# Optimization experiments

Measured on AMD Instinct MI355X. Metric: run time of the kernel, lower is better.

The kernel has to match this reference:

```python
import jax, jax.numpy as jnp
import numpy as np

DEPTH = 6
DIM = 512
HEADS = 8
HD = DIM // HEADS          # head_dim = 64
HALF = HD // 4             # RoPE2D half_dim = 16
N = 85                     # 1 CLS + 4 + 16 + 64
TOKENS = [1, 4, 16, 64]
MAX_FREQ = 10.0
NEG = -1e30


def _build_mask():
    bounds = np.cumsum([0] + TOKENS)
    M = np.array([[1, 0, 0, 1], [1, 1, 0, 0], [1, 0, 1, 0], [0, 0, 0, 1]])
    m = np.full((N, N), NEG, np.float32)
    for i in range(4):
        for j in range(4):
            if M[i, j]:
                m[bounds[i]:bounds[i + 1], bounds[j]:bounds[j + 1]] = 0.0
    return jnp.asarray(m)

MASK = _build_mask()
FREQS = jnp.exp(jnp.arange(HALF, dtype=jnp.float32) * (-np.log(MAX_FREQ) / HALF))


def _centers():
    allc = []
    for g in (2, 4, 8):
        step = 1.0 / g
        off = step / 2
        ys, xs = np.meshgrid(np.arange(g), np.arange(g), indexing='ij')
        c = np.stack([off + xs * step, off + ys * step], axis=-1).reshape(-1, 2)
        allc.append(c)
    return jnp.asarray(np.concatenate(allc, 0), dtype=jnp.float32)


def _ln(x, w, b):
    mu = x.mean(-1, keepdims=True)
    var = x.var(-1, keepdims=True)
    return (x - mu) / jnp.sqrt(var + 1e-5) * w + b


def _rope(t, coords):
    # t: [B, H, M, HD] patch tokens (CLS excluded); coords: [M, 2]
    two_pi = 2.0 * jnp.pi
    ang_x = coords[:, 0:1] * FREQS[None, :] * two_pi   # [M, HALF]
    ang_y = coords[:, 1:2] * FREQS[None, :] * two_pi
    cx, sx = jnp.cos(ang_x), jnp.sin(ang_x)
    cy, sy = jnp.cos(ang_y), jnp.sin(ang_y)
    t = t.reshape(t.shape[:-1] + (4, HALF))
    x0, x1, x2, x3 = t[..., 0, :], t[..., 1, :], t[..., 2, :], t[..., 3, :]
    r = jnp.stack([x0 * cx - x1 * sx, x0 * sx + x1 * cx,
                   x2 * cy - x3 * sy, x2 * sy + x3 * cy], axis=-2)
    return r.reshape(r.shape[:-2] + (HD,))


def _attn(x, coords, qkv_w, qkv_b, proj_w, proj_b):
    B = x.shape[0]
    qkv = (x @ qkv_w + qkv_b).reshape(B, N, 3, HEADS, HD).transpose(2, 0, 3, 1, 4)
    q, k, v = qkv[0], qkv[1], qkv[2]   # each [B, H, N, HD]
    q = jnp.concatenate([q[:, :, :1], _rope(q[:, :, 1:], coords)], axis=2)
    k = jnp.concatenate([k[:, :, :1], _rope(k[:, :, 1:], coords)], axis=2)
    scores = jnp.einsum('bhqd,bhkd->bhqk', q, k) * (HD ** -0.5) + MASK
    a = jax.nn.softmax(scores, axis=-1)
    out = jnp.einsum('bhqk,bhkd->bhqd', a, v).transpose(0, 2, 1, 3).reshape(B, N, DIM)
    return out @ proj_w + proj_b


def _forward(x, coords, ln1_w, ln1_b, qkv_w, qkv_b, proj_w, proj_b,
             ln2_w, ln2_b, fc1_w, fc1_b, fc2_w, fc2_b, lnf_w, lnf_b):
    for l in range(DEPTH):
        h = _ln(x, ln1_w[l], ln1_b[l])
        x = x + _attn(h, coords, qkv_w[l], qkv_b[l], proj_w[l], proj_b[l])
        h = _ln(x, ln2_w[l], ln2_b[l])
        h = jax.nn.gelu(h @ fc1_w[l] + fc1_b[l], approximate=False)  # torch nn.GELU = erf
        x = x + h @ fc2_w[l] + fc2_b[l]
    return _ln(x, lnf_w, lnf_b)


def setup_inputs() -> dict:
    key = jax.random.key(0)
    ks = jax.random.split(key, 5)
    B = 512
    def w(k, shape, s=0.02):
        return jax.random.normal(k, shape, jnp.float32) * s
    return {
        'x': jax.random.normal(ks[0], (B, N, DIM), jnp.float32),
        'coords': _centers(),
        'ln1_w': jnp.ones((DEPTH, DIM), jnp.float32),
        'ln1_b': jnp.zeros((DEPTH, DIM), jnp.float32),
        'qkv_w': w(ks[1], (DEPTH, DIM, 3 * DIM)),
        'qkv_b': jnp.zeros((DEPTH, 3 * DIM), jnp.float32),
        'proj_w': w(ks[2], (DEPTH, DIM, DIM)),
        'proj_b': jnp.zeros((DEPTH, DIM), jnp.float32),
        'ln2_w': jnp.ones((DEPTH, DIM), jnp.float32),
        'ln2_b': jnp.zeros((DEPTH, DIM), jnp.float32),
        'fc1_w': w(ks[3], (DEPTH, DIM, 4 * DIM)),
        'fc1_b': jnp.zeros((DEPTH, 4 * DIM), jnp.float32),
        'fc2_w': w(ks[4], (DEPTH, 4 * DIM, DIM)),
        'fc2_b': jnp.zeros((DEPTH, DIM), jnp.float32),
        'lnf_w': jnp.ones((DIM,), jnp.float32),
        'lnf_b': jnp.zeros((DIM,), jnp.float32),
    }


def reference(x, coords, ln1_w, ln1_b, qkv_w, qkv_b, proj_w, proj_b,
              ln2_w, ln2_b, fc1_w, fc1_b, fc2_w, fc2_b, lnf_w, lnf_b):
    return _forward(x, coords, ln1_w, ln1_b, qkv_w, qkv_b, proj_w, proj_b,
                    ln2_w, ln2_b, fc1_w, fc1_b, fc2_w, fc2_b, lnf_w, lnf_b)
```

## Files before the change

kernel.cpp:

```cpp
#include <hip/hip_runtime.h>
#include <hip/hip_bf16.h>

typedef unsigned short u16;
typedef unsigned int u32;
typedef __attribute__((ext_vector_type(8))) short short8;
typedef __attribute__((ext_vector_type(4))) float floatx4;

#define MTOT 43520
#define DIMM 512
#define NHEAD 8

__device__ __forceinline__ float b2f(u16 u) { return __uint_as_float(((unsigned)u) << 16); }
__device__ __forceinline__ u16 f2b(float f) {
  unsigned u = __float_as_uint(f);
  return (u16)((u + 0x7FFFu + ((u >> 16) & 1u)) >> 16);
}

__device__ __forceinline__ void gld16(void* lds, const void* g) {
  __builtin_amdgcn_global_load_lds(
      (const __attribute__((address_space(1))) u32*)g,
      (__attribute__((address_space(3))) u32*)lds, 16, 0, 0);
}

__global__ __launch_bounds__(256) void transpose_conv(const float* __restrict__ in,
    u16* __restrict__ out, int K, int N)
{
  const float* W  = in  + (size_t)blockIdx.z * K * N;
  u16*         Wt = out + (size_t)blockIdx.z * K * N;
  int n0 = blockIdx.x * 64, k0 = blockIdx.y * 64;
  int t = threadIdx.x;
  #pragma unroll
  for (int i = 0; i < 2; i++) {
    int task = t + i * 256;
    int n = task >> 3, kc = (task & 7) * 8;
    u16 tmp[8];
    #pragma unroll
    for (int j = 0; j < 8; j++)
      tmp[j] = f2b(W[(size_t)(k0 + kc + j) * N + n0 + n]);
    *(uint4*)&Wt[(size_t)(n0 + n) * K + k0 + kc] = *(uint4*)tmp;
  }
}

template<int OUTF32>
__global__ __launch_bounds__(256) void ln_kernel(const float* __restrict__ x,
    const float* __restrict__ w, const float* __restrict__ b, void* __restrict__ out)
{
  int row  = blockIdx.x * 4 + (threadIdx.x >> 6);
  int lane = threadIdx.x & 63;
  const float* xr = x + (size_t)row * DIMM;
  float4 a = ((const float4*)xr)[lane * 2];
  float4 c = ((const float4*)xr)[lane * 2 + 1];
  float f[8] = { a.x, a.y, a.z, a.w, c.x, c.y, c.z, c.w };

  float s = 0.f, ss = 0.f;
  #pragma unroll
  for (int i = 0; i < 8; i++) { s += f[i]; ss += f[i] * f[i]; }
  #pragma unroll
  for (int off = 32; off > 0; off >>= 1) {
    s  += __shfl_xor(s,  off);
    ss += __shfl_xor(ss, off);
  }
  float mu  = s * (1.f / 512.f);
  float var = ss * (1.f / 512.f) - mu * mu;
  float rs  = rsqrtf(var + 1e-5f);

  float4 w0 = ((const float4*)w)[lane * 2], w1 = ((const float4*)w)[lane * 2 + 1];
  float4 b0 = ((const float4*)b)[lane * 2], b1 = ((const float4*)b)[lane * 2 + 1];
  float wv[8] = { w0.x, w0.y, w0.z, w0.w, w1.x, w1.y, w1.z, w1.w };
  float bv[8] = { b0.x, b0.y, b0.z, b0.w, b1.x, b1.y, b1.z, b1.w };

  if (OUTF32) {
    float res[8];
    #pragma unroll
    for (int i = 0; i < 8; i++) res[i] = (f[i] - mu) * rs * wv[i] + bv[i];
    float* orow = (float*)out + (size_t)row * DIMM;
    ((float4*)orow)[lane * 2]     = *(float4*)&res[0];
    ((float4*)orow)[lane * 2 + 1] = *(float4*)&res[4];
  } else {
    u16 res[8];
    #pragma unroll
    for (int i = 0; i < 8; i++) res[i] = f2b((f[i] - mu) * rs * wv[i] + bv[i]);
    ((uint4*)((u16*)out + (size_t)row * DIMM))[lane] = *(uint4*)res;
  }
}

template<int EPI>
__global__ __launch_bounds__(256) void gemm_nt(
    const u16* __restrict__ A, const u16* __restrict__ Bt,
    const float* __restrict__ bias, const float* __restrict__ resid,
    void* __restrict__ Cv, int Nd, int K)
{
  __shared__ u16 As[128 * 32];
  __shared__ u16 Bs[128 * 32];

  int t = threadIdx.x;
  int m0 = blockIdx.y * 128, n0 = blockIdx.x * 128;
  int wave = t >> 6, lane = t & 63, quad = lane >> 4, l16 = lane & 15;
  int wr = wave >> 1, wc = wave & 1;

  floatx4 zero = {0.f, 0.f, 0.f, 0.f};
  floatx4 acc[4][4];
  #pragma unroll
  for (int mt = 0; mt < 4; mt++)
    #pragma unroll
    for (int nt = 0; nt < 4; nt++) acc[mt][nt] = zero;

  int srow = wave * 32 + (lane >> 2);
  int kch  = (lane & 3) * 8;

  for (int k0 = 0; k0 < K; k0 += 32) {
    #pragma unroll
    for (int i = 0; i < 2; i++) {
      int row = srow + i * 16;
      gld16(&As[(wave * 32 + i * 16) * 32], A  + (size_t)(m0 + row) * K + k0 + kch);
      gld16(&Bs[(wave * 32 + i * 16) * 32], Bt + (size_t)(n0 + row) * K + k0 + kch);
    }
    __syncthreads();

    short8 af[4];
    #pragma unroll
    for (int mt = 0; mt < 4; mt++)
      af[mt] = *(const short8*)&As[(wr * 64 + mt * 16 + l16) * 32 + quad * 8];
    #pragma unroll
    for (int nt = 0; nt < 4; nt++) {
      short8 bf = *(const short8*)&Bs[(wc * 64 + nt * 16 + l16) * 32 + quad * 8];
      #pragma unroll
      for (int mt = 0; mt < 4; mt++)
        acc[mt][nt] = __builtin_amdgcn_mfma_f32_16x16x32_bf16(af[mt], bf, acc[mt][nt], 0, 0, 0);
    }
    __syncthreads();
  }

  #pragma unroll
  for (int mt = 0; mt < 4; mt++) {
    #pragma unroll
    for (int nt = 0; nt < 4; nt++) {
      int nc = n0 + wc * 64 + nt * 16 + l16;
      float bv = bias[nc];
      #pragma unroll
      for (int r = 0; r < 4; r++) {
        int mr = m0 + wr * 64 + mt * 16 + quad * 4 + r;
        size_t idx = (size_t)mr * Nd + nc;
        float v = acc[mt][nt][r] + bv;
        if constexpr (EPI == 1) {
          ((float*)Cv)[idx] = v + resid[idx];
        } else if constexpr (EPI == 2) {
          v = 0.5f * v * (1.f + erff(v * 0.70710678118654752f));
          ((u16*)Cv)[idx] = f2b(v);
        } else {
          ((u16*)Cv)[idx] = f2b(v);
        }
      }
    }
  }
}

__device__ __forceinline__ int grp(int tk) { return tk == 0 ? 0 : (tk < 5 ? 1 : (tk < 21 ? 2 : 3)); }

__global__ __launch_bounds__(256) void attn_kernel(const u16* __restrict__ qkv,
    const float* __restrict__ coords, u16* __restrict__ out)
{
  __shared__ u16 Qs[96 * 72];
  __shared__ u16 Ks[96 * 72];
  __shared__ u16 Vt[64 * 104];
  __shared__ u16 Pb[96 * 104];

  int b = blockIdx.x >> 3, h = blockIdx.x & 7;
  int tid = threadIdx.x;
  const u16* base = qkv + ((size_t)b * 85) * 1536 + h * 64;

  for (int idx = tid; idx < 96 * 64; idx += 256) {
    int tk = idx >> 6, d = idx & 63;
    float qv = 0.f, kv = 0.f; u16 vv = 0;
    if (tk < 85) {
      const u16* qp = base + (size_t)tk * 1536;
      vv = qp[1024 + d];
      if (tk == 0) {
        qv = b2f(qp[d]); kv = b2f(qp[512 + d]);
      } else {
        int j = d & 15, q4 = d >> 4;
        float coord = coords[(tk - 1) * 2 + (q4 >> 1)];
        float freq = __expf((float)j * -0.14391156831212787f);
        float ang = coord * freq * 6.283185307179586f;
        float sn, cs; __sincosf(ang, &sn, &cs);
        int p0 = ((q4 & 2) << 4) + j, p1 = p0 + 16;
        float a0 = b2f(qp[p0]),       a1 = b2f(qp[p1]);
        float k0 = b2f(qp[512 + p0]), k1 = b2f(qp[512 + p1]);
        if (q4 & 1) { qv = a0 * sn + a1 * cs; kv = k0 * sn + k1 * cs; }
        else        { qv = a0 * cs - a1 * sn; kv = k0 * cs - k1 * sn; }
      }
    }
    Qs[tk * 72 + d] = f2b(qv);
    Ks[tk * 72 + d] = f2b(kv);
    Vt[d * 104 + tk] = vv;
  }
  __syncthreads();

  int wave = tid >> 6, lane = tid & 63, quad = lane >> 4, l16 = lane & 15;
  const unsigned MBITS = 0x8539u;
  floatx4 zero = {0.f, 0.f, 0.f, 0.f};

  int nb = (wave < 2) ? 2 : 1;
  for (int bi = 0; bi < nb; bi++) {
    int band = (bi == 0) ? wave : wave + 4;

    short8 a0 = *(const short8*)&Qs[(band * 16 + l16) * 72 + quad * 8];
    short8 a1 = *(const short8*)&Qs[(band * 16 + l16) * 72 + 32 + quad * 8];
    floatx4 s[6];
    #pragma unroll
    for (int nt = 0; nt < 6; nt++) {
      short8 b0 = *(const short8*)&Ks[(nt * 16 + l16) * 72 + quad * 8];
      short8 b1 = *(const short8*)&Ks[(nt * 16 + l16) * 72 + 32 + quad * 8];
      floatx4 tmp = __builtin_amdgcn_mfma_f32_16x16x32_bf16(a0, b0, zero, 0, 0, 0);
      s[nt] = __builtin_amdgcn_mfma_f32_16x16x32_bf16(a1, b1, tmp, 0, 0, 0);
    }

    int rb = band * 16 + quad * 4;
    #pragma unroll
    for (int r = 0; r < 4; r++) {
      int row = rb + r, gr = grp(row);
      float mx = -3.4e38f;
      #pragma unroll
      for (int nt = 0; nt < 6; nt++) {
        int col = nt * 16 + l16;
        float m = (col < 85 && ((MBITS >> (gr * 4 + grp(col))) & 1)) ? 0.f : -1e30f;
        s[nt][r] = s[nt][r] * 0.125f + m;
        mx = fmaxf(mx, s[nt][r]);
      }
      #pragma unroll
      for (int off = 1; off < 16; off <<= 1) mx = fmaxf(mx, __shfl_xor(mx, off));
      float sum = 0.f;
      #pragma unroll
      for (int nt = 0; nt < 6; nt++) { s[nt][r] = __expf(s[nt][r] - mx); sum += s[nt][r]; }
      #pragma unroll
      for (int off = 1; off < 16; off <<= 1) sum += __shfl_xor(sum, off);
      float inv = 1.f / sum;
      #pragma unroll
      for (int nt = 0; nt < 6; nt++)
        Pb[row * 104 + nt * 16 + l16] = f2b(s[nt][r] * inv);
    }

    floatx4 o[4];
    #pragma unroll
    for (int nt2 = 0; nt2 < 4; nt2++) o[nt2] = zero;
    #pragma unroll
    for (int ks = 0; ks < 3; ks++) {
      short8 pa = *(const short8*)&Pb[(band * 16 + l16) * 104 + ks * 32 + quad * 8];
      #pragma unroll
      for (int nt2 = 0; nt2 < 4; nt2++) {
        short8 vb = *(const short8*)&Vt[(nt2 * 16 + l16) * 104 + ks * 32 + quad * 8];
        o[nt2] = __builtin_amdgcn_mfma_f32_16x16x32_bf16(pa, vb, o[nt2], 0, 0, 0);
      }
    }
    #pragma unroll
    for (int nt2 = 0; nt2 < 4; nt2++) {
      #pragma unroll
      for (int r = 0; r < 4; r++) {
        int row = rb + r;
        if (row < 85)
          out[((size_t)b * 85 + row) * 512 + h * 64 + nt2 * 16 + l16] = f2b(o[nt2][r]);
      }
    }
  }
}

extern "C" void kernel_launch(void* const* d_in, const int* in_sizes, int n_in,
                              void* d_out, int out_size, void* d_ws, size_t ws_size,
                              hipStream_t stream) {
  (void)in_sizes; (void)n_in; (void)out_size; (void)ws_size;
  const float* x_in   = (const float*)d_in[0];
  const float* coords = (const float*)d_in[1];
  const float* ln1_w  = (const float*)d_in[2];
  const float* ln1_b  = (const float*)d_in[3];
  const float* qkv_w  = (const float*)d_in[4];
  const float* qkv_b  = (const float*)d_in[5];
  const float* proj_w = (const float*)d_in[6];
  const float* proj_b = (const float*)d_in[7];
  const float* ln2_w  = (const float*)d_in[8];
  const float* ln2_b  = (const float*)d_in[9];
  const float* fc1_w  = (const float*)d_in[10];
  const float* fc1_b  = (const float*)d_in[11];
  const float* fc2_w  = (const float*)d_in[12];
  const float* fc2_b  = (const float*)d_in[13];
  const float* lnf_w  = (const float*)d_in[14];
  const float* lnf_b  = (const float*)d_in[15];

  float* xb = (float*)d_ws;
  u16*   hb = (u16*)(xb + (size_t)MTOT * 512);
  u16*   qb = hb + (size_t)MTOT * 512;
  u16*   wbuf = qb + (size_t)MTOT * 2048;
  u16* wq = wbuf;
  u16* wp = wq + (size_t)6 * 512 * 1536;
  u16* w1 = wp + (size_t)6 * 512 * 512;
  u16* w2 = w1 + (size_t)6 * 512 * 2048;

  dim3 blk(256);
  transpose_conv<<<dim3(1536 / 64, 512 / 64, 6), blk, 0, stream>>>(qkv_w, wq, 512, 1536);
  transpose_conv<<<dim3(512 / 64, 512 / 64, 6), blk, 0, stream>>>(proj_w, wp, 512, 512);
  transpose_conv<<<dim3(2048 / 64, 512 / 64, 6), blk, 0, stream>>>(fc1_w, w1, 512, 2048);
  transpose_conv<<<dim3(512 / 64, 2048 / 64, 6), blk, 0, stream>>>(fc2_w, w2, 2048, 512);

  for (int l = 0; l < 6; l++) {
    const float* xcur = (l == 0) ? x_in : xb;
    ln_kernel<0><<<MTOT / 4, blk, 0, stream>>>(xcur, ln1_w + l * 512, ln1_b + l * 512, hb);
    gemm_nt<0><<<dim3(1536 / 128, MTOT / 128), blk, 0, stream>>>(
        hb, wq + (size_t)l * 512 * 1536, qkv_b + (size_t)l * 1536, nullptr, qb, 1536, 512);
    attn_kernel<<<512 * NHEAD, blk, 0, stream>>>(qb, coords, hb);
    gemm_nt<1><<<dim3(512 / 128, MTOT / 128), blk, 0, stream>>>(
        hb, wp + (size_t)l * 512 * 512, proj_b + (size_t)l * 512, xcur, xb, 512, 512);
    ln_kernel<0><<<MTOT / 4, blk, 0, stream>>>(xb, ln2_w + l * 512, ln2_b + l * 512, hb);
    gemm_nt<2><<<dim3(2048 / 128, MTOT / 128), blk, 0, stream>>>(
        hb, w1 + (size_t)l * 512 * 2048, fc1_b + (size_t)l * 2048, nullptr, qb, 2048, 512);
    gemm_nt<1><<<dim3(512 / 128, MTOT / 128), blk, 0, stream>>>(
        qb, w2 + (size_t)l * 2048 * 512, fc2_b + (size_t)l * 512, xb, xb, 512, 2048);
  }
  ln_kernel<1><<<MTOT / 4, blk, 0, stream>>>(xb, lnf_w, lnf_b, d_out);
}
```

Before: 4.386 ms.

## Replace 128x128 GEMM with 256x256 double-buffered, swizzled, XCD-remapped MFMA kernel

Result: faster. 4.240 ms (-3.3%).

```diff
diff --git a/kernel.cpp b/kernel.cpp
--- a/kernel.cpp
+++ b/kernel.cpp
@@ -85,61 +85,150 @@
 }
 
 template<int EPI>
-__global__ __launch_bounds__(256) void gemm_nt(
+__global__ __launch_bounds__(512, 2) void gemm256(
     const u16* __restrict__ A, const u16* __restrict__ Bt,
     const float* __restrict__ bias, const float* __restrict__ resid,
-    void* __restrict__ Cv, int Nd, int K)
+    void* __restrict__ Cv, int Nd, int K, int gx)
 {
-  __shared__ u16 As[128 * 32];
-  __shared__ u16 Bs[128 * 32];
+  __shared__ u16 As[2][2][128][64];
+  __shared__ u16 Bs[2][2][128][64];
+
+  int nwg  = gridDim.x;
+  int orig = blockIdx.x;
+  int xcd = orig & 7, cidx = orig >> 3;
+  int qq = nwg >> 3, rr8 = nwg & 7;
+  int nid = (xcd < rr8 ? xcd * (qq + 1) : rr8 * (qq + 1) + (xcd - rr8) * qq) + cidx;
+  int bx = nid % gx, by = nid / gx;
+  int m0 = by * 256, n0 = bx * 256;
 
   int t = threadIdx.x;
-  int m0 = blockIdx.y * 128, n0 = blockIdx.x * 128;
-  int wave = t >> 6, lane = t & 63, quad = lane >> 4, l16 = lane & 15;
-  int wr = wave >> 1, wc = wave & 1;
+  int w = t >> 6, l = t & 63;
+  int wr = w >> 2, wc = w & 3, quad = l >> 4, l16 = l & 15;
+  int KT = K >> 6;
+
+  int Rb = 8 * w + (l >> 3);
+  int slog8 = (((l & 7) ^ ((l >> 3) & 7)) << 3);
+  const u16* gAm = A  + (size_t)m0 * K + slog8;
+  const u16* gBn = Bt + (size_t)n0 * K + slog8;
+  int sx = l16 & 7;
+
+  auto STAGE = [&](int ktj, int h) {
+    int c = ktj & 1;
+    u16* lb = (h < 2) ? &As[c][h & 1][0][0] : &Bs[c][h & 1][0][0];
+    const u16* g = ((h < 2) ? gAm : gBn) + (size_t)((h & 1) * 128 + Rb) * K + ktj * 64;
+    gld16(lb + w * 512,       g);
+    gld16(lb + (8 + w) * 512, g + (size_t)64 * K);
+  };
+
+  STAGE(0, 0); STAGE(0, 1); STAGE(0, 2); STAGE(0, 3);
+  STAGE(1, 0); STAGE(1, 1);
+  asm volatile("s_waitcnt vmcnt(4)" ::: "memory");
+  __builtin_amdgcn_s_barrier();
+  __builtin_amdgcn_sched_barrier(0);
 
   floatx4 zero = {0.f, 0.f, 0.f, 0.f};
-  floatx4 acc[4][4];
+  floatx4 acc[8][4];
   #pragma unroll
-  for (int mt = 0; mt < 4; mt++)
+  for (int mt = 0; mt < 8; mt++)
     #pragma unroll
     for (int nt = 0; nt < 4; nt++) acc[mt][nt] = zero;
 
-  int srow = wave * 32 + (lane >> 2);
-  int kch  = (lane & 3) * 8;
-
-  for (int k0 = 0; k0 < K; k0 += 32) {
-    #pragma unroll
-    for (int i = 0; i < 2; i++) {
-      int row = srow + i * 16;
-      gld16(&As[(wave * 32 + i * 16) * 32], A  + (size_t)(m0 + row) * K + k0 + kch);
-      gld16(&Bs[(wave * 32 + i * 16) * 32], Bt + (size_t)(n0 + row) * K + k0 + kch);
-    }
-    __syncthreads();
-
-    short8 af[4];
+  for (int kt = 0; kt < KT; ++kt) {
+    int c = kt & 1;
+    const u16 (*Ah)[64] = As[c][wr];
+    const u16 (*Bh)[64] = Bs[c][wc >> 1];
+    int bl = (wc & 1) * 64;
+
+    short8 af[8][2], bf[4][2];
+
     #pragma unroll
     for (int mt = 0; mt < 4; mt++)
-      af[mt] = *(const short8*)&As[(wr * 64 + mt * 16 + l16) * 32 + quad * 8];
-    #pragma unroll
-    for (int nt = 0; nt < 4; nt++) {
-      short8 bf = *(const short8*)&Bs[(wc * 64 + nt * 16 + l16) * 32 + quad * 8];
+      #pragma unroll
+      for (int kk = 0; kk < 2; kk++)
+        af[mt][kk] = *(const short8*)&Ah[mt * 16 + l16][((kk * 4 + quad) ^ sx) << 3];
+    #pragma unroll
+    for (int nt = 0; nt < 2; nt++)
+      #pragma unroll
+      for (int kk = 0; kk < 2; kk++)
+        bf[nt][kk] = *(const short8*)&Bh[bl + nt * 16 + l16][((kk * 4 + quad) ^ sx) << 3];
+    { int j = 4 * kt + 6; if (j < 4 * KT) STAGE(j >> 2, j & 3); }
+    __builtin_amdgcn_s_barrier();
+    __builtin_amdgcn_s_setprio(1);
+    #pragma unroll
+    for (int nt = 0; nt < 2; nt++)
       #pragma unroll
       for (int mt = 0; mt < 4; mt++)
-        acc[mt][nt] = __builtin_amdgcn_mfma_f32_16x16x32_bf16(af[mt], bf, acc[mt][nt], 0, 0, 0);
-    }
-    __syncthreads();
+        #pragma unroll
+        for (int kk = 0; kk < 2; kk++)
+          acc[mt][nt] = __builtin_amdgcn_mfma_f32_16x16x32_bf16(af[mt][kk], bf[nt][kk], acc[mt][nt], 0, 0, 0);
+    __builtin_amdgcn_s_setprio(0);
+    __builtin_amdgcn_s_barrier();
+
+    #pragma unroll
+    for (int mt = 4; mt < 8; mt++)
+      #pragma unroll
+      for (int kk = 0; kk < 2; kk++)
+        af[mt][kk] = *(const short8*)&Ah[mt * 16 + l16][((kk * 4 + quad) ^ sx) << 3];
+    #pragma unroll
+    for (int nt = 2; nt < 4; nt++)
+      #pragma unroll
+      for (int kk = 0; kk < 2; kk++)
+        bf[nt][kk] = *(const short8*)&Bh[bl + nt * 16 + l16][((kk * 4 + quad) ^ sx) << 3];
+    { int j = 4 * kt + 7; if (j < 4 * KT) STAGE(j >> 2, j & 3); }
+    __builtin_amdgcn_s_barrier();
+    __builtin_amdgcn_s_setprio(1);
+    #pragma unroll
+    for (int nt = 2; nt < 4; nt++)
+      #pragma unroll
+      for (int mt = 4; mt < 8; mt++)
+        #pragma unroll
+        for (int kk = 0; kk < 2; kk++)
+          acc[mt][nt] = __builtin_amdgcn_mfma_f32_16x16x32_bf16(af[mt][kk], bf[nt][kk], acc[mt][nt], 0, 0, 0);
+    __builtin_amdgcn_s_setprio(0);
+    __builtin_amdgcn_s_barrier();
+
+    { int j = 4 * kt + 8; if (j < 4 * KT) STAGE(j >> 2, j & 3); }
+    __builtin_amdgcn_s_barrier();
+    __builtin_amdgcn_s_setprio(1);
+    #pragma unroll
+    for (int nt = 2; nt < 4; nt++)
+      #pragma unroll
+      for (int mt = 0; mt < 4; mt++)
+        #pragma unroll
+        for (int kk = 0; kk < 2; kk++)
+          acc[mt][nt] = __builtin_amdgcn_mfma_f32_16x16x32_bf16(af[mt][kk], bf[nt][kk], acc[mt][nt], 0, 0, 0);
+    __builtin_amdgcn_s_setprio(0);
+    __builtin_amdgcn_s_barrier();
+
+    { int j = 4 * kt + 9; if (j < 4 * KT) STAGE(j >> 2, j & 3); }
+    __builtin_amdgcn_s_barrier();
+    __builtin_amdgcn_s_setprio(1);
+    #pragma unroll
+    for (int nt = 0; nt < 2; nt++)
+      #pragma unroll
+      for (int mt = 4; mt < 8; mt++)
+        #pragma unroll
+        for (int kk = 0; kk < 2; kk++)
+          acc[mt][nt] = __builtin_amdgcn_mfma_f32_16x16x32_bf16(af[mt][kk], bf[nt][kk], acc[mt][nt], 0, 0, 0);
+    __builtin_amdgcn_s_setprio(0);
+
+    if (kt < KT - 1) {
+      if (kt == KT - 2) asm volatile("s_waitcnt vmcnt(0)" ::: "memory");
+      else              asm volatile("s_waitcnt vmcnt(4)" ::: "memory");
+      __builtin_amdgcn_s_barrier();
+      __builtin_amdgcn_sched_barrier(0);
+    }
   }
 
   #pragma unroll
-  for (int mt = 0; mt < 4; mt++) {
+  for (int mt = 0; mt < 8; mt++) {
     #pragma unroll
     for (int nt = 0; nt < 4; nt++) {
       int nc = n0 + wc * 64 + nt * 16 + l16;
       float bv = bias[nc];
       #pragma unroll
       for (int r = 0; r < 4; r++) {
-        int mr = m0 + wr * 64 + mt * 16 + quad * 4 + r;
+        int mr = m0 + wr * 128 + mt * 16 + quad * 4 + r;
         size_t idx = (size_t)mr * Nd + nc;
         float v = acc[mt][nt][r] + bv;
         if constexpr (EPI == 1) {
@@ -295,24 +384,26 @@
   u16* w2 = w1 + (size_t)6 * 512 * 2048;
 
   dim3 blk(256);
+  dim3 blkg(512);
   transpose_conv<<<dim3(1536 / 64, 512 / 64, 6), blk, 0, stream>>>(qkv_w, wq, 512, 1536);
   transpose_conv<<<dim3(512 / 64, 512 / 64, 6), blk, 0, stream>>>(proj_w, wp, 512, 512);
   transpose_conv<<<dim3(2048 / 64, 512 / 64, 6), blk, 0, stream>>>(fc1_w, w1, 512, 2048);
   transpose_conv<<<dim3(512 / 64, 2048 / 64, 6), blk, 0, stream>>>(fc2_w, w2, 2048, 512);
 
+  const int MT = MTOT / 256;
   for (int l = 0; l < 6; l++) {
     const float* xcur = (l == 0) ? x_in : xb;
     ln_kernel<0><<<MTOT / 4, blk, 0, stream>>>(xcur, ln1_w + l * 512, ln1_b + l * 512, hb);
-    gemm_nt<0><<<dim3(1536 / 128, MTOT / 128), blk, 0, stream>>>(
-        hb, wq + (size_t)l * 512 * 1536, qkv_b + (size_t)l * 1536, nullptr, qb, 1536, 512);
+    gemm256<0><<<6 * MT, blkg, 0, stream>>>(
+        hb, wq + (size_t)l * 512 * 1536, qkv_b + (size_t)l * 1536, nullptr, qb, 1536, 512, 6);
     attn_kernel<<<512 * NHEAD, blk, 0, stream>>>(qb, coords, hb);
-    gemm_nt<1><<<dim3(512 / 128, MTOT / 128), blk, 0, stream>>>(
-        hb, wp + (size_t)l * 512 * 512, proj_b + (size_t)l * 512, xcur, xb, 512, 512);
+    gemm256<1><<<2 * MT, blkg, 0, stream>>>(
+        hb, wp + (size_t)l * 512 * 512, proj_b + (size_t)l * 512, xcur, xb, 512, 512, 2);
     ln_kernel<0><<<MTOT / 4, blk, 0, stream>>>(xb, ln2_w + l * 512, ln2_b + l * 512, hb);
-    gemm_nt<2><<<dim3(2048 / 128, MTOT / 128), blk, 0, stream>>>(
-        hb, w1 + (size_t)l * 512 * 2048, fc1_b + (size_t)l * 2048, nullptr, qb, 2048, 512);
-    gemm_nt<1><<<dim3(512 / 128, MTOT / 128), blk, 0, stream>>>(
-        qb, w2 + (size_t)l * 2048 * 512, fc2_b + (size_t)l * 512, xb, xb, 512, 2048);
+    gemm256<2><<<8 * MT, blkg, 0, stream>>>(
+        hb, w1 + (size_t)l * 512 * 2048, fc1_b + (size_t)l * 2048, nullptr, qb, 2048, 512, 8);
+    gemm256<1><<<2 * MT, blkg, 0, stream>>>(
+        qb, w2 + (size_t)l * 2048 * 512, fc2_b + (size_t)l * 512, xb, xb, 512, 2048, 2);
   }
   ln_kernel<1><<<MTOT / 4, blk, 0, stream>>>(xb, lnf_w, lnf_b, d_out);
 }
```
